# Performance work log

Hardware: AMD Instinct MI355X
Metric: run time of the kernel (lower is better)

Reference implementation:

```python
import jax, jax.numpy as jnp
import numpy as np

CHUNK = 256
ROPE_BASE = 10000.0
EPS = 1e-6


def setup_inputs() -> dict:
    key = jax.random.key(0)
    ks = jax.random.split(key, 8)
    B, N, D, H, K = 4, 8192, 1024, 16, 4
    x = jax.random.normal(ks[0], (B, N, D), dtype=jnp.float32)
    norm_scale = jnp.ones((D,), dtype=jnp.float32)
    conv_w = jax.random.normal(ks[1], (D, 1, K), dtype=jnp.float32) * 0.2
    conv_b = jax.random.normal(ks[2], (D,), dtype=jnp.float32) * 0.02
    in_proj_w = jax.random.normal(ks[3], (D, 3 * D), dtype=jnp.float32) * 0.02
    dt_bias = jax.random.normal(ks[4], (D,), dtype=jnp.float32) * 0.5
    head_mix = jnp.eye(H, dtype=jnp.float32) + 0.02 * jax.random.normal(ks[5], (H, H), dtype=jnp.float32)
    out_proj_w = jax.random.normal(ks[6], (D, D), dtype=jnp.float32) * 0.02
    return {"x": x, "norm_scale": norm_scale, "conv_w": conv_w, "conv_b": conv_b,
            "in_proj_w": in_proj_w, "dt_bias": dt_bias, "head_mix": head_mix,
            "out_proj_w": out_proj_w}


def _rmsnorm(x, scale):
    xf = x.astype(jnp.float32)
    rms = jax.lax.rsqrt(jnp.mean(xf * xf, axis=-1, keepdims=True) + EPS)
    out = scale.astype(jnp.float32) * (xf * rms)
    return jnp.clip(out, -60000.0, 60000.0).astype(x.dtype)


def _rope(v, N, d_head, dtype):
    # v: (B, N, H, d_head); cos/sin: (N, d_head//2)
    half = d_head // 2
    inv_freq = 1.0 / (ROPE_BASE ** (jnp.arange(0, d_head, 2, dtype=jnp.float32) / d_head))
    freqs = jnp.arange(N, dtype=jnp.float32)[:, None] * inv_freq[None, :]
    cos = jnp.cos(freqs).astype(dtype)[None, :, None, :]
    sin = jnp.sin(freqs).astype(dtype)[None, :, None, :]
    v1, v2 = v[..., :half], v[..., half:]
    return jnp.concatenate([v1 * cos - v2 * sin, v1 * sin + v2 * cos], axis=-1)


def reference(x, norm_scale, conv_w, conv_b, in_proj_w, dt_bias, head_mix, out_proj_w):
    residual = x
    B, N, D = x.shape
    H = head_mix.shape[0]
    d_head = D // H
    xn = _rmsnorm(x, norm_scale)

    # depthwise causal conv: torch pads K-1 both sides then truncates to N -> left-pad only
    K = conv_w.shape[-1]
    xc = jax.lax.conv_general_dilated(
        xn.transpose(0, 2, 1), conv_w, window_strides=(1,), padding=[(K - 1, 0)],
        feature_group_count=D, dimension_numbers=("NCH", "OIH", "NCH"))
    xc = (xc + conv_b[None, :, None]).transpose(0, 2, 1)  # (B, N, D)
    xc = xc * jax.nn.sigmoid(xc)  # SiLU

    fused = xc @ in_proj_w  # (B, N, 3D)
    dt_raw, v, gate_raw = jnp.split(fused, 3, axis=-1)
    dt = jnp.clip(jax.nn.softplus(dt_raw.astype(jnp.float32) + dt_bias.astype(jnp.float32)),
                  0.001, 2.0).astype(dt_raw.dtype)
    gate = jax.nn.sigmoid(gate_raw)
    log_alpha = -dt.astype(jnp.float32)

    v_rot = _rope(v.reshape(B, N, H, d_head), N, d_head, x.dtype).reshape(B, N, D)
    v_in = (v_rot * dt).astype(jnp.float32)

    # pad to multiple of CHUNK (static)
    pad = (-N) % CHUNK
    if pad:
        v_in = jnp.pad(v_in, ((0, 0), (0, pad), (0, 0)))
        log_alpha = jnp.pad(log_alpha, ((0, 0), (0, pad), (0, 0)))
    Np = N + pad
    nc = Np // CHUNK
    v_ch = v_in.reshape(B, nc, CHUNK, D)
    la_ch = log_alpha.reshape(B, nc, CHUNK, D)

    # intra-chunk stabilized cumulative scan
    L = jnp.clip(jnp.cumsum(la_ch, axis=2), -20.0, 0.0)
    L_max = jnp.max(L, axis=2, keepdims=True)
    L_st = L - L_max
    cum_scaled = jnp.cumsum(jnp.exp(-L_st) * v_ch, axis=2)
    chunk_out = jnp.exp(L_st) * cum_scaled  # (B, nc, CHUNK, D)

    if nc > 1:
        # inter-chunk carry, fully parallel
        bdecay = L[:, :, -1, :]            # (B, nc, D)
        bout = chunk_out[:, :, -1, :]      # (B, nc, D)
        cum_decay = jnp.clip(jnp.cumsum(bdecay, axis=1), -80.0, 0.0)
        stab = jnp.max(cum_decay, axis=1, keepdims=True)
        ncd = jnp.clip(cum_decay - stab, -20.0, 0.0)
        seeds = bout * jnp.exp(-ncd)
        shifted = jnp.pad(seeds[:, :-1], ((0, 0), (1, 0), (0, 0)))
        carries = jnp.cumsum(shifted, axis=1) * jnp.exp(ncd)  # (B, nc, D)
        final = chunk_out + carries[:, :, None, :] * jnp.exp(L)
    else:
        final = chunk_out
    final = final.astype(x.dtype).reshape(B, Np, D)[:, :N, :]

    v_mix = jnp.einsum("bnhd,hm->bnmd", final.reshape(B, N, H, d_head), head_mix)
    final = v_mix.reshape(B, N, D)
    out = (final * gate) @ out_proj_w
    return residual + out
```

## Files before the change

kernel.cpp:

```cpp
#include <hip/hip_runtime.h>

#define TOK 32768
#define DMODEL 1024
#define NSEQ 8192
#define NCHK 32
#define CHUNKC 256
#define KDIM 1024
#define LOG2E 1.44269504f

typedef __attribute__((ext_vector_type(8))) short bf16x8;
typedef __attribute__((ext_vector_type(4))) float f32x4;

__device__ __forceinline__ unsigned short f2bf(float f) {
  unsigned u = __float_as_uint(f);
  u += 0x7fffu + ((u >> 16) & 1u);
  return (unsigned short)(u >> 16);
}
__device__ __forceinline__ float bf2f(unsigned short h) {
  return __uint_as_float(((unsigned)h) << 16);
}
__device__ __forceinline__ float sigm(float x) {
  return __builtin_amdgcn_rcpf(1.f + exp2f(-LOG2E * x));
}

typedef __attribute__((address_space(3))) unsigned int lds_u32_t;
typedef const __attribute__((address_space(1))) unsigned int glb_u32_t;

__device__ __forceinline__ void gl_lds16(const void* g, void* l) {
  __builtin_amdgcn_global_load_lds((glb_u32_t*)g, (lds_u32_t*)l, 16, 0, 0);
}

__global__ __launch_bounds__(256) void prep_k(const float* __restrict__ w1,
                                              const float* __restrict__ w2,
                                              unsigned short* __restrict__ w1t,
                                              unsigned short* __restrict__ w2t,
                                              float2* __restrict__ tab) {
  __shared__ float tile[32][33];
  const int bid = blockIdx.x;
  const int t = threadIdx.x;
  if (bid < 4096) {
    const float* in;
    unsigned short* out;
    int c0, r0;
    if (bid < 3072) { in = w1; out = w1t; c0 = (bid % 96) * 32; r0 = (bid / 96) * 32; }
    else            { in = w2; out = w2t; c0 = ((bid - 3072) & 31) * 32; r0 = ((bid - 3072) >> 5) * 32; }
    const int C = (bid < 3072) ? 3072 : 1024;
    const int tx = t & 31, ty = t >> 5;
#pragma unroll
    for (int i = 0; i < 32; i += 8)
      tile[ty + i][tx] = in[(long)(r0 + ty + i) * C + c0 + tx];
    __syncthreads();
#pragma unroll
    for (int i = 0; i < 32; i += 8)
      out[(long)(c0 + ty + i) * 1024 + r0 + tx] = f2bf(tile[tx][ty + i]);
  } else {
    const int i = (bid - 4096) * 256 + t;
    const int f = i & 31, n = i >> 5;
    const float invf = exp2f(-(float)f * (13.287712379549449f / 32.0f));
    const float ang = (float)n * invf;
    tab[i] = make_float2(cosf(ang), sinf(ang));
  }
}

__global__ __launch_bounds__(256) void rmsconv_k(const float* __restrict__ x,
                                                 const float* __restrict__ scale,
                                                 const float* __restrict__ w,
                                                 const float* __restrict__ cb,
                                                 unsigned short* __restrict__ xc) {
  __shared__ float red[11][4];
  const int t = threadIdx.x;
  const long row0 = (long)blockIdx.x * 8;
  const bool seqstart = ((row0 & (NSEQ - 1)) == 0);
  const float4 sc = ((const float4*)scale)[t];
  float4 vr[11];
#pragma unroll
  for (int i = 0; i < 11; ++i) {
    if (i < 3 && seqstart) {
      vr[i] = make_float4(0.f, 0.f, 0.f, 0.f);
    } else {
      vr[i] = ((const float4*)(x + (row0 - 3 + i) * DMODEL))[t];
    }
    float ss = vr[i].x * vr[i].x + vr[i].y * vr[i].y + vr[i].z * vr[i].z + vr[i].w * vr[i].w;
#pragma unroll
    for (int off = 32; off > 0; off >>= 1) ss += __shfl_down(ss, off);
    if ((t & 63) == 0) red[i][t >> 6] = ss;
  }
  __syncthreads();
#pragma unroll
  for (int i = 0; i < 11; ++i) {
    const float tot = red[i][0] + red[i][1] + red[i][2] + red[i][3];
    const float rr = rsqrtf(tot * (1.0f / DMODEL) + 1e-6f);
    vr[i].x = fminf(fmaxf(vr[i].x * rr * sc.x, -60000.f), 60000.f);
    vr[i].y = fminf(fmaxf(vr[i].y * rr * sc.y, -60000.f), 60000.f);
    vr[i].z = fminf(fmaxf(vr[i].z * rr * sc.z, -60000.f), 60000.f);
    vr[i].w = fminf(fmaxf(vr[i].w * rr * sc.w, -60000.f), 60000.f);
  }
  const int d0 = t * 4;
  float wl[4][4];
#pragma unroll
  for (int j = 0; j < 4; ++j) {
    const float4 t4 = *(const float4*)(w + (d0 + j) * 4);
    wl[j][0] = t4.x; wl[j][1] = t4.y; wl[j][2] = t4.z; wl[j][3] = t4.w;
  }
  const float4 cb4 = ((const float4*)cb)[t];
#pragma unroll
  for (int orow = 0; orow < 8; ++orow) {
    float o[4] = {0.f, 0.f, 0.f, 0.f};
#pragma unroll
    for (int k = 0; k < 4; ++k) {
      const float4 xv = vr[orow + k];
      o[0] += xv.x * wl[0][k]; o[1] += xv.y * wl[1][k];
      o[2] += xv.z * wl[2][k]; o[3] += xv.w * wl[3][k];
    }
    ushort4 st;
    { const float a = o[0] + cb4.x; st.x = f2bf(a * sigm(a)); }
    { const float a = o[1] + cb4.y; st.y = f2bf(a * sigm(a)); }
    { const float a = o[2] + cb4.z; st.z = f2bf(a * sigm(a)); }
    { const float a = o[3] + cb4.w; st.w = f2bf(a * sigm(a)); }
    *(ushort4*)(xc + (row0 + orow) * DMODEL + d0) = st;
  }
}

template <int EPI, int NBN, int SBN>
__global__ __launch_bounds__(512) void gemm_bt(const unsigned short* __restrict__ A,
                                               const unsigned short* __restrict__ BT,
                                               unsigned short* __restrict__ ob,
                                               float* __restrict__ of,
                                               const float* __restrict__ resid) {
  __shared__ unsigned short As[3][8192];
  __shared__ unsigned short Bs[3][8192];
  const int tid = threadIdx.x;
  const int l = tid & 63;
  const int w = tid >> 6;
  const int wr = w >> 2, wc = w & 3;
  constexpr int NC = (EPI == 0) ? 3072 : 1024;
  constexpr int NKT = KDIM / 32;

  constexpr int BPS = 4 * SBN;
  constexpr int NBNS = NBN / SBN;
  const int lin = blockIdx.y * NBN + blockIdx.x;
  const int xcd = lin & 7;
  const int g = lin >> 3;
  const int s = g / BPS;
  const int r = g - s * BPS;
  const int bmo = r / SBN;
  const int bno = r - bmo * SBN;
  const int bmS = s / NBNS;
  const int bnS = s - bmS * NBNS;
  const int bm = xcd * 16 + bmS * 4 + bmo;
  const int bn = bnS * SBN + bno;

  f32x4 acc[8][4];
#pragma unroll
  for (int m = 0; m < 8; ++m)
#pragma unroll
    for (int n = 0; n < 4; ++n) acc[m][n] = {0.f, 0.f, 0.f, 0.f};

  const int srcc = (((l & 3) ^ ((l >> 3) & 3)) * 8);
  const unsigned short* aG0 = A + ((long)(bm * 256 + w * 32 + (l >> 2))) * KDIM + srcc;
  const unsigned short* bG0 = BT + ((long)(bn * 256 + w * 32 + (l >> 2))) * KDIM + srcc;
  const int wL0 = w * 1024;

#define STAGE(buf, k0)                                          \
  { gl_lds16(aG0 + (k0),            &As[buf][wL0]);             \
    gl_lds16(aG0 + (k0) + 16*KDIM,  &As[buf][wL0 + 512]);       \
    gl_lds16(bG0 + (k0),            &Bs[buf][wL0]);             \
    gl_lds16(bG0 + (k0) + 16*KDIM,  &Bs[buf][wL0 + 512]); }

  const int eoff = (((l >> 4) ^ ((l >> 1) & 3)) * 8);
  const int aRowOff = (wr * 128 + (l & 15)) * 32 + eoff;
  const int bRowOff = (wc * 64 + (l & 15)) * 32 + eoff;

  auto compute = [&](int cur) {
    const unsigned short* Ab = &As[cur][0];
    const unsigned short* Bb = &Bs[cur][0];
    bf16x8 af[8], bfr[4];
#pragma unroll
    for (int m = 0; m < 8; ++m) af[m] = *(const bf16x8*)&Ab[aRowOff + m * 512];
#pragma unroll
    for (int n = 0; n < 4; ++n) bfr[n] = *(const bf16x8*)&Bb[bRowOff + n * 512];
    __builtin_amdgcn_s_setprio(1);
#pragma unroll
    for (int m = 0; m < 8; ++m)
#pragma unroll
      for (int n = 0; n < 4; ++n)
        acc[m][n] = __builtin_amdgcn_mfma_f32_16x16x32_bf16(af[m], bfr[n], acc[m][n], 0, 0, 0);
    __builtin_amdgcn_s_setprio(0);
  };

  STAGE(0, 0);
  STAGE(1, 32);
  asm volatile("s_waitcnt vmcnt(4)" ::: "memory");
  int cur = 0, nxt = 2;
  for (int t = 0; t < NKT - 2; ++t) {
    __builtin_amdgcn_s_barrier();
    __builtin_amdgcn_sched_barrier(0);
    STAGE(nxt, (t + 2) * 32);
    compute(cur);
    asm volatile("s_waitcnt vmcnt(4)" ::: "memory");
    cur = (cur == 2) ? 0 : cur + 1;
    nxt = (nxt == 2) ? 0 : nxt + 1;
  }
  __builtin_amdgcn_s_barrier();
  __builtin_amdgcn_sched_barrier(0);
  compute(cur);
  asm volatile("s_waitcnt vmcnt(0)" ::: "memory");
  cur = (cur == 2) ? 0 : cur + 1;
  __builtin_amdgcn_s_barrier();
  __builtin_amdgcn_sched_barrier(0);
  compute(cur);
#undef STAGE

  const int rbase = bm * 256 + wr * 128;
  const int cbase = bn * 256 + wc * 64;
  const int lr4 = (l >> 4) * 4;
  const int lc16 = l & 15;

  if constexpr (EPI == 0) {
#pragma unroll
    for (int m = 0; m < 8; ++m)
#pragma unroll
      for (int n = 0; n < 4; ++n) {
        const int col = cbase + n * 16 + lc16;
#pragma unroll
        for (int j2 = 0; j2 < 4; ++j2) {
          const int row = rbase + m * 16 + lr4 + j2;
          ob[(long)row * NC + col] = f2bf(acc[m][n][j2]);
        }
      }
  } else {
#pragma unroll
    for (int m = 0; m < 8; ++m)
#pragma unroll
      for (int n = 0; n < 4; ++n) {
        const int col = cbase + n * 16 + lc16;
#pragma unroll
        for (int j2 = 0; j2 < 4; ++j2) {
          const int row = rbase + m * 16 + lr4 + j2;
          const long o = (long)row * NC + col;
          of[o] = resid[o] + acc[m][n][j2];
        }
      }
  }
}

__global__ __launch_bounds__(256) void scan1_k(const unsigned short* __restrict__ fu,
                                               const float* __restrict__ dt_bias,
                                               const float2* __restrict__ tab,
                                               float* __restrict__ Llast,
                                               float* __restrict__ bout) {
  const int idx = blockIdx.x * 256 + threadIdx.x;
  const int d = idx & 1023;
  const int ch = (idx >> 10) & 31;
  const int b = idx >> 15;
  const long base = ((long)b * NSEQ + ch * CHUNKC) * 3072 + d;
  const float bias = dt_bias[d];
  const int f = d & 31;
  const bool hi = (d & 32) != 0;
  const int po = hi ? -32 : 32;
  float run = 0.f, s = 0.f, L = 0.f;
#pragma unroll 4
  for (int c = 0; c < CHUNKC; ++c) {
    const long o = base + (long)c * 3072;
    const float a = bf2f(fu[o]) + bias;
    const float e2 = exp2f(-LOG2E * fabsf(a));
    const float sp = fmaxf(a, 0.f) + 0.69314718f * log2f(1.f + e2);
    const float dtv = fminf(fmaxf(sp, 0.001f), 2.0f);
    const float own = bf2f(fu[o + 1024]);
    const float oth = bf2f(fu[o + 1024 + po]);
    const float2 cs = tab[(ch * CHUNKC + c) * 32 + f];
    const float vr = own * cs.x + (hi ? oth * cs.y : -oth * cs.y);
    run -= dtv;
    L = fminf(fmaxf(run, -20.f), 0.f);
    s += exp2f(-LOG2E * L) * (vr * dtv);
  }
  Llast[idx] = L;
  bout[idx] = exp2f(LOG2E * L) * s;
}

__global__ __launch_bounds__(256) void scan2_k(const float* __restrict__ Llast,
                                               const float* __restrict__ bout,
                                               float* __restrict__ carry) {
  const int idx = blockIdx.x * 256 + threadIdx.x;
  const int d = idx & 1023;
  const int b = idx >> 10;
  const long base = (long)b * (NCHK * DMODEL) + d;
  float cd[NCHK];
  float run = 0.f, stab = -1e30f;
#pragma unroll
  for (int ch = 0; ch < NCHK; ++ch) {
    run += Llast[base + ch * DMODEL];
    cd[ch] = fminf(fmaxf(run, -80.f), 0.f);
    stab = fmaxf(stab, cd[ch]);
  }
  float acc = 0.f;
#pragma unroll
  for (int ch = 0; ch < NCHK; ++ch) {
    const float ncd = fminf(fmaxf(cd[ch] - stab, -20.f), 0.f);
    carry[base + ch * DMODEL] = acc * exp2f(LOG2E * ncd);
    acc += bout[base + ch * DMODEL] * exp2f(-LOG2E * ncd);
  }
}

__global__ __launch_bounds__(256) void scan3_k(unsigned short* fu,
                                               const float* __restrict__ dt_bias,
                                               const float2* __restrict__ tab,
                                               const float* __restrict__ carry) {
  const int idx = blockIdx.x * 256 + threadIdx.x;
  const int d = idx & 1023;
  const int ch = (idx >> 10) & 31;
  const int b = idx >> 15;
  const long base = ((long)b * NSEQ + ch * CHUNKC) * 3072 + d;
  const float bias = dt_bias[d];
  const int f = d & 31;
  const bool hi = (d & 32) != 0;
  const int po = hi ? -32 : 32;
  const float ce = carry[idx];
  float run = 0.f, s = 0.f;
#pragma unroll 4
  for (int c = 0; c < CHUNKC; ++c) {
    const long o = base + (long)c * 3072;
    const float a = bf2f(fu[o]) + bias;
    const float e2 = exp2f(-LOG2E * fabsf(a));
    const float sp = fmaxf(a, 0.f) + 0.69314718f * log2f(1.f + e2);
    const float dtv = fminf(fmaxf(sp, 0.001f), 2.0f);
    const float own = bf2f(fu[o + 1024]);
    const float oth = bf2f(fu[o + 1024 + po]);
    const float2 cs = tab[(ch * CHUNKC + c) * 32 + f];
    const float vr = own * cs.x + (hi ? oth * cs.y : -oth * cs.y);
    run -= dtv;
    const float L = fminf(fmaxf(run, -20.f), 0.f);
    s += exp2f(-LOG2E * L) * (vr * dtv);
    fu[o + 1024] = f2bf(exp2f(LOG2E * L) * (s + ce));
  }
}

__global__ __launch_bounds__(256) void headmix_k(const unsigned short* __restrict__ fu,
                                                 const float* __restrict__ hm,
                                                 unsigned short* __restrict__ A2) {
  __shared__ float mixs[256];
  const int t = threadIdx.x;
  mixs[t] = hm[t];
  __syncthreads();
  const long row = (long)blockIdx.x * 4 + (t >> 6);
  const int dd = t & 63;
  const unsigned short* fv0 = fu + row * 3072 + 1024 + dd;
  const unsigned short* gv0 = fu + row * 3072 + 2048 + dd;
  float fv[16];
#pragma unroll
  for (int h = 0; h < 16; ++h) fv[h] = bf2f(fv0[h * 64]);
#pragma unroll
  for (int m = 0; m < 16; ++m) {
    float o = 0.f;
#pragma unroll
    for (int h = 0; h < 16; ++h) o += fv[h] * mixs[h * 16 + m];
    A2[row * DMODEL + m * 64 + dd] = f2bf(o * sigm(bf2f(gv0[m * 64])));
  }
}

extern "C" void kernel_launch(void* const* d_in, const int* in_sizes, int n_in,
                              void* d_out, int out_size, void* d_ws, size_t ws_size,
                              hipStream_t stream) {
  const float* x        = (const float*)d_in[0];
  const float* nscale   = (const float*)d_in[1];
  const float* conv_w   = (const float*)d_in[2];
  const float* conv_b   = (const float*)d_in[3];
  const float* in_proj  = (const float*)d_in[4];
  const float* dt_bias  = (const float*)d_in[5];
  const float* head_mix = (const float*)d_in[6];
  const float* out_proj = (const float*)d_in[7];
  float* out = (float*)d_out;

  char* p = (char*)d_ws;
  unsigned short* W1T = (unsigned short*)p; p += (size_t)3072 * 1024 * 2;
  unsigned short* W2T = (unsigned short*)p; p += (size_t)1024 * 1024 * 2;
  float2* tab  = (float2*)p; p += (size_t)NSEQ * 32 * sizeof(float2);
  float* Llast = (float*)p;  p += (size_t)131072 * 4;
  float* bout  = (float*)p;  p += (size_t)131072 * 4;
  float* carry = (float*)p;  p += (size_t)131072 * 4;
  unsigned short* fusedb = (unsigned short*)p; p += (size_t)TOK * 3072 * 2;
  unsigned short* xc     = (unsigned short*)p; p += (size_t)TOK * DMODEL * 2;

  prep_k<<<5120, 256, 0, stream>>>(in_proj, out_proj, W1T, W2T, tab);
  rmsconv_k<<<TOK / 8, 256, 0, stream>>>(x, nscale, conv_w, conv_b, xc);

  gemm_bt<0, 12, 6><<<dim3(12, 128), 512, 0, stream>>>(xc, W1T, fusedb, nullptr, nullptr);
  scan1_k<<<512, 256, 0, stream>>>(fusedb, dt_bias, tab, Llast, bout);
  scan2_k<<<16, 256, 0, stream>>>(Llast, bout, carry);
  scan3_k<<<512, 256, 0, stream>>>(fusedb, dt_bias, tab, carry);
  headmix_k<<<TOK / 4, 256, 0, stream>>>(fusedb, head_mix, xc );
  gemm_bt<1, 4, 4><<<dim3(4, 128), 512, 0, stream>>>(xc, W2T, nullptr, out, x);
}
```

Baseline: 654.4 us.

## Split chunk scans into parallel segments and shrink GEMM tile to 128x256

The scan kernels now divide each 256-step chunk into four 64-step segments handled by separate waves. Segment decay sums and partial scan sums are combined through shared memory, which exposes four times more parallelism for the serial, latency-bound loops. Scan3 recomputes the segment pass twice in exchange. The GEMMs move to 256-thread blocks with 128x256 tiles and a doubled grid, trading operand reuse for more blocks and occupancy.

```diff
diff --git a/kernel.cpp b/kernel.cpp
--- a/kernel.cpp
+++ b/kernel.cpp
@@ -122,17 +122,16 @@
 }
 
 template <int EPI, int NBN, int SBN>
-__global__ __launch_bounds__(512) void gemm_bt(const unsigned short* __restrict__ A,
+__global__ __launch_bounds__(256) void gemm_bt(const unsigned short* __restrict__ A,
                                                const unsigned short* __restrict__ BT,
                                                unsigned short* __restrict__ ob,
                                                float* __restrict__ of,
                                                const float* __restrict__ resid) {
-  __shared__ unsigned short As[3][8192];
-  __shared__ unsigned short Bs[3][8192];
+  __shared__ unsigned short As[3][128 * 32];
+  __shared__ unsigned short Bs[3][256 * 32];
   const int tid = threadIdx.x;
   const int l = tid & 63;
   const int w = tid >> 6;
-  const int wr = w >> 2, wc = w & 3;
   constexpr int NC = (EPI == 0) ? 3072 : 1024;
   constexpr int NKT = KDIM / 32;
 
@@ -147,7 +146,7 @@
   const int bno = r - bmo * SBN;
   const int bmS = s / NBNS;
   const int bnS = s - bmS * NBNS;
-  const int bm = xcd * 16 + bmS * 4 + bmo;
+  const int bm = xcd * 32 + bmS * 4 + bmo;
   const int bn = bnS * SBN + bno;
 
   f32x4 acc[8][4];
@@ -157,28 +156,33 @@
     for (int n = 0; n < 4; ++n) acc[m][n] = {0.f, 0.f, 0.f, 0.f};
 
   const int srcc = (((l & 3) ^ ((l >> 3) & 3)) * 8);
-  const unsigned short* aG0 = A + ((long)(bm * 256 + w * 32 + (l >> 2))) * KDIM + srcc;
-  const unsigned short* bG0 = BT + ((long)(bn * 256 + w * 32 + (l >> 2))) * KDIM + srcc;
-  const int wL0 = w * 1024;
-
-#define STAGE(buf, k0)                                          \
-  { gl_lds16(aG0 + (k0),            &As[buf][wL0]);             \
-    gl_lds16(aG0 + (k0) + 16*KDIM,  &As[buf][wL0 + 512]);       \
-    gl_lds16(bG0 + (k0),            &Bs[buf][wL0]);             \
-    gl_lds16(bG0 + (k0) + 16*KDIM,  &Bs[buf][wL0 + 512]); }
+  const unsigned short* aG0 = A + ((long)(bm * 128 + w * 32 + (l >> 2))) * KDIM + srcc;
+  const unsigned short* bG0 = BT + ((long)(bn * 256 + w * 64 + (l >> 2))) * KDIM + srcc;
+  const int aLo = (w * 32) * 32;
+  const int bLo = (w * 64) * 32;
+
+#define STAGE(buf, k0)                                           \
+  {                                                              \
+    gl_lds16(aG0 + (k0),             &As[buf][aLo]);             \
+    gl_lds16(aG0 + (k0) + 16 * KDIM, &As[buf][aLo + 512]);       \
+    gl_lds16(bG0 + (k0),             &Bs[buf][bLo]);             \
+    gl_lds16(bG0 + (k0) + 16 * KDIM, &Bs[buf][bLo + 512]);       \
+    gl_lds16(bG0 + (k0) + 32 * KDIM, &Bs[buf][bLo + 1024]);      \
+    gl_lds16(bG0 + (k0) + 48 * KDIM, &Bs[buf][bLo + 1536]);      \
+  }
 
   const int eoff = (((l >> 4) ^ ((l >> 1) & 3)) * 8);
-  const int aRowOff = (wr * 128 + (l & 15)) * 32 + eoff;
-  const int bRowOff = (wc * 64 + (l & 15)) * 32 + eoff;
+  const int arow0 = (l & 15) * 32 + eoff;
+  const int brow0 = (w * 64 + (l & 15)) * 32 + eoff;
 
   auto compute = [&](int cur) {
     const unsigned short* Ab = &As[cur][0];
     const unsigned short* Bb = &Bs[cur][0];
     bf16x8 af[8], bfr[4];
 #pragma unroll
-    for (int m = 0; m < 8; ++m) af[m] = *(const bf16x8*)&Ab[aRowOff + m * 512];
-#pragma unroll
-    for (int n = 0; n < 4; ++n) bfr[n] = *(const bf16x8*)&Bb[bRowOff + n * 512];
+    for (int m = 0; m < 8; ++m) af[m] = *(const bf16x8*)&Ab[arow0 + m * 512];
+#pragma unroll
+    for (int n = 0; n < 4; ++n) bfr[n] = *(const bf16x8*)&Bb[brow0 + n * 512];
     __builtin_amdgcn_s_setprio(1);
 #pragma unroll
     for (int m = 0; m < 8; ++m)
@@ -190,14 +194,14 @@
 
   STAGE(0, 0);
   STAGE(1, 32);
-  asm volatile("s_waitcnt vmcnt(4)" ::: "memory");
+  asm volatile("s_waitcnt vmcnt(6)" ::: "memory");
   int cur = 0, nxt = 2;
   for (int t = 0; t < NKT - 2; ++t) {
     __builtin_amdgcn_s_barrier();
     __builtin_amdgcn_sched_barrier(0);
     STAGE(nxt, (t + 2) * 32);
     compute(cur);
-    asm volatile("s_waitcnt vmcnt(4)" ::: "memory");
+    asm volatile("s_waitcnt vmcnt(6)" ::: "memory");
     cur = (cur == 2) ? 0 : cur + 1;
     nxt = (nxt == 2) ? 0 : nxt + 1;
   }
@@ -211,8 +215,8 @@
   compute(cur);
 #undef STAGE
 
-  const int rbase = bm * 256 + wr * 128;
-  const int cbase = bn * 256 + wc * 64;
+  const int rbase = bm * 128;
+  const int cbase = bn * 256 + w * 64;
   const int lr4 = (l >> 4) * 4;
   const int lc16 = l & 15;
 
@@ -249,33 +253,55 @@
                                                const float2* __restrict__ tab,
                                                float* __restrict__ Llast,
                                                float* __restrict__ bout) {
-  const int idx = blockIdx.x * 256 + threadIdx.x;
-  const int d = idx & 1023;
-  const int ch = (idx >> 10) & 31;
-  const int b = idx >> 15;
-  const long base = ((long)b * NSEQ + ch * CHUNKC) * 3072 + d;
+  __shared__ float Ssum[4][64];
+  __shared__ float Ssca[4][64];
+  const int t = threadIdx.x;
+  const int lane = t & 63, seg = t >> 6;
+  const int cid = blockIdx.x * 64 + lane;
+  const int d = cid & 1023;
+  const int ch = (cid >> 10) & 31;
+  const int b = cid >> 15;
+  const long base = ((long)b * NSEQ + ch * CHUNKC + seg * 64) * 3072 + d;
   const float bias = dt_bias[d];
   const int f = d & 31;
   const bool hi = (d & 32) != 0;
   const int po = hi ? -32 : 32;
-  float run = 0.f, s = 0.f, L = 0.f;
-#pragma unroll 4
-  for (int c = 0; c < CHUNKC; ++c) {
-    const long o = base + (long)c * 3072;
-    const float a = bf2f(fu[o]) + bias;
+  float dtv[64];
+  float segsum = 0.f;
+#pragma unroll
+  for (int i = 0; i < 64; ++i) {
+    const float a = bf2f(fu[base + (long)i * 3072]) + bias;
     const float e2 = exp2f(-LOG2E * fabsf(a));
     const float sp = fmaxf(a, 0.f) + 0.69314718f * log2f(1.f + e2);
-    const float dtv = fminf(fmaxf(sp, 0.001f), 2.0f);
+    dtv[i] = fminf(fmaxf(sp, 0.001f), 2.0f);
+    segsum += dtv[i];
+  }
+  Ssum[seg][lane] = segsum;
+  __syncthreads();
+  float basev = 0.f;
+  for (int k = 0; k < seg; ++k) basev -= Ssum[k][lane];
+  const int posbase = ch * CHUNKC + seg * 64;
+  float run = basev, s = 0.f;
+#pragma unroll
+  for (int i = 0; i < 64; ++i) {
+    const long o = base + (long)i * 3072;
     const float own = bf2f(fu[o + 1024]);
     const float oth = bf2f(fu[o + 1024 + po]);
-    const float2 cs = tab[(ch * CHUNKC + c) * 32 + f];
+    const float2 cs = tab[(posbase + i) * 32 + f];
     const float vr = own * cs.x + (hi ? oth * cs.y : -oth * cs.y);
-    run -= dtv;
-    L = fminf(fmaxf(run, -20.f), 0.f);
-    s += exp2f(-LOG2E * L) * (vr * dtv);
-  }
-  Llast[idx] = L;
-  bout[idx] = exp2f(LOG2E * L) * s;
+    run -= dtv[i];
+    const float L = fminf(fmaxf(run, -20.f), 0.f);
+    s += exp2f(-LOG2E * L) * (vr * dtv[i]);
+  }
+  Ssca[seg][lane] = s;
+  __syncthreads();
+  if (seg == 0) {
+    const float tot = Ssum[0][lane] + Ssum[1][lane] + Ssum[2][lane] + Ssum[3][lane];
+    const float Ll = fminf(fmaxf(-tot, -20.f), 0.f);
+    const float st = Ssca[0][lane] + Ssca[1][lane] + Ssca[2][lane] + Ssca[3][lane];
+    Llast[cid] = Ll;
+    bout[cid] = exp2f(LOG2E * Ll) * st;
+  }
 }
 
 __global__ __launch_bounds__(256) void scan2_k(const float* __restrict__ Llast,
@@ -306,31 +332,62 @@
                                                const float* __restrict__ dt_bias,
                                                const float2* __restrict__ tab,
                                                const float* __restrict__ carry) {
-  const int idx = blockIdx.x * 256 + threadIdx.x;
-  const int d = idx & 1023;
-  const int ch = (idx >> 10) & 31;
-  const int b = idx >> 15;
-  const long base = ((long)b * NSEQ + ch * CHUNKC) * 3072 + d;
+  __shared__ float Ssum[4][64];
+  __shared__ float Ssca[4][64];
+  const int t = threadIdx.x;
+  const int lane = t & 63, seg = t >> 6;
+  const int cid = blockIdx.x * 64 + lane;
+  const int d = cid & 1023;
+  const int ch = (cid >> 10) & 31;
+  const int b = cid >> 15;
+  const long base = ((long)b * NSEQ + ch * CHUNKC + seg * 64) * 3072 + d;
   const float bias = dt_bias[d];
   const int f = d & 31;
   const bool hi = (d & 32) != 0;
   const int po = hi ? -32 : 32;
-  const float ce = carry[idx];
-  float run = 0.f, s = 0.f;
-#pragma unroll 4
-  for (int c = 0; c < CHUNKC; ++c) {
-    const long o = base + (long)c * 3072;
-    const float a = bf2f(fu[o]) + bias;
+  const float ce = carry[cid];
+  float dtv[64];
+  float segsum = 0.f;
+#pragma unroll
+  for (int i = 0; i < 64; ++i) {
+    const float a = bf2f(fu[base + (long)i * 3072]) + bias;
     const float e2 = exp2f(-LOG2E * fabsf(a));
     const float sp = fmaxf(a, 0.f) + 0.69314718f * log2f(1.f + e2);
-    const float dtv = fminf(fmaxf(sp, 0.001f), 2.0f);
+    dtv[i] = fminf(fmaxf(sp, 0.001f), 2.0f);
+    segsum += dtv[i];
+  }
+  Ssum[seg][lane] = segsum;
+  __syncthreads();
+  float basev = 0.f;
+  for (int k = 0; k < seg; ++k) basev -= Ssum[k][lane];
+  const int posbase = ch * CHUNKC + seg * 64;
+  float run = basev, s = 0.f;
+#pragma unroll
+  for (int i = 0; i < 64; ++i) {
+    const long o = base + (long)i * 3072;
     const float own = bf2f(fu[o + 1024]);
     const float oth = bf2f(fu[o + 1024 + po]);
-    const float2 cs = tab[(ch * CHUNKC + c) * 32 + f];
+    const float2 cs = tab[(posbase + i) * 32 + f];
     const float vr = own * cs.x + (hi ? oth * cs.y : -oth * cs.y);
-    run -= dtv;
+    run -= dtv[i];
     const float L = fminf(fmaxf(run, -20.f), 0.f);
-    s += exp2f(-LOG2E * L) * (vr * dtv);
+    s += exp2f(-LOG2E * L) * (vr * dtv[i]);
+  }
+  Ssca[seg][lane] = s;
+  __syncthreads();
+  float sbase = 0.f;
+  for (int k = 0; k < seg; ++k) sbase += Ssca[k][lane];
+  run = basev; s = sbase;
+#pragma unroll
+  for (int i = 0; i < 64; ++i) {
+    const long o = base + (long)i * 3072;
+    const float own = bf2f(fu[o + 1024]);
+    const float oth = bf2f(fu[o + 1024 + po]);
+    const float2 cs = tab[(posbase + i) * 32 + f];
+    const float vr = own * cs.x + (hi ? oth * cs.y : -oth * cs.y);
+    run -= dtv[i];
+    const float L = fminf(fmaxf(run, -20.f), 0.f);
+    s += exp2f(-LOG2E * L) * (vr * dtv[i]);
     fu[o + 1024] = f2bf(exp2f(LOG2E * L) * (s + ce));
   }
 }
@@ -384,10 +441,10 @@
   prep_k<<<5120, 256, 0, stream>>>(in_proj, out_proj, W1T, W2T, tab);
   rmsconv_k<<<TOK / 8, 256, 0, stream>>>(x, nscale, conv_w, conv_b, xc);
 
-  gemm_bt<0, 12, 6><<<dim3(12, 128), 512, 0, stream>>>(xc, W1T, fusedb, nullptr, nullptr);
-  scan1_k<<<512, 256, 0, stream>>>(fusedb, dt_bias, tab, Llast, bout);
+  gemm_bt<0, 12, 6><<<dim3(12, 256), 256, 0, stream>>>(xc, W1T, fusedb, nullptr, nullptr);
+  scan1_k<<<2048, 256, 0, stream>>>(fusedb, dt_bias, tab, Llast, bout);
   scan2_k<<<16, 256, 0, stream>>>(Llast, bout, carry);
-  scan3_k<<<512, 256, 0, stream>>>(fusedb, dt_bias, tab, carry);
+  scan3_k<<<2048, 256, 0, stream>>>(fusedb, dt_bias, tab, carry);
   headmix_k<<<TOK / 4, 256, 0, stream>>>(fusedb, head_mix, xc );
-  gemm_bt<1, 4, 4><<<dim3(4, 128), 512, 0, stream>>>(xc, W2T, nullptr, out, x);
-}
+  gemm_bt<1, 4, 4><<<dim3(4, 256), 256, 0, stream>>>(xc, W2T, nullptr, out, x);
+}
```

New measurement: 787.0 us. +20.3%, slower.
